# Performance work log

Measured on AMD Instinct MI355X. Metric: run time of the kernel, lower is better.

## Reference

```python
import jax, jax.numpy as jnp
import numpy as np
import math

D_MODEL = 512
N_HEADS = 8
PATH_LEN = 3
B, L, S = 4, 1024, 1024


def _path_index_structure(L, S, path_length):
    """Precompute the static multi-hop index structure (numpy, trace-time)."""
    i = np.arange(L)[:, None]          # [L,1]
    j = np.arange(S)[None, :]          # [1,S]
    step = (j - i) / path_length       # float
    # Python int() truncates toward zero; i + k*step >= 0 here, so floor == int().
    m1 = np.floor(i + 1 * step).astype(np.int32)  # [L,S] first intermediate point
    m2 = np.floor(i + 2 * step).astype(np.int32)  # [L,S] second intermediate point
    near = np.abs(i - j) <= path_length            # [L,S] bool: direct-score region
    return m1, m2, near


def setup_inputs() -> dict:
    key = jax.random.key(0)
    ks = jax.random.split(key, 7)
    inp = {
        "queries": jax.random.normal(ks[0], (B, L, D_MODEL), dtype=jnp.float32),
        "keys": jax.random.normal(ks[1], (B, S, D_MODEL), dtype=jnp.float32),
        "values": jax.random.normal(ks[2], (B, S, D_MODEL), dtype=jnp.float32),
        # nn.Linear(d_model, d_keys*n_heads, bias=False): stored as [in, out] so y = x @ W
        "W_q": jax.random.normal(ks[3], (D_MODEL, D_MODEL), dtype=jnp.float32) * 0.02,
        "W_k": jax.random.normal(ks[4], (D_MODEL, D_MODEL), dtype=jnp.float32) * 0.02,
        "W_v": jax.random.normal(ks[5], (D_MODEL, D_MODEL), dtype=jnp.float32) * 0.02,
        "W_o": jax.random.normal(ks[6], (D_MODEL, D_MODEL), dtype=jnp.float32) * 0.02,
    }
    return inp


def reference(queries, keys, values, W_q, W_k, W_v, W_o):
    Bv, Lv, _ = queries.shape
    Sv = keys.shape[1]
    H = N_HEADS
    q = (queries @ W_q).reshape(Bv, Lv, H, -1).transpose(0, 2, 1, 3)  # [B,H,L,D]
    k = (keys @ W_k).reshape(Bv, Sv, H, -1).transpose(0, 2, 1, 3)     # [B,H,S,D]
    v = (values @ W_v).reshape(Bv, Sv, H, -1).transpose(0, 2, 1, 3)   # [B,H,S,D]
    D = q.shape[-1]

    scores = jnp.einsum('bhld,bhsd->bhls', q, k) / math.sqrt(D)  # [B,H,L,S]

    # --- path-score modification (vectorized form of the nested loops) ---
    m1, m2, near = _path_index_structure(Lv, Sv, PATH_LEN)
    row = np.arange(Lv)[:, None]
    col = np.arange(Sv)[None, :]
    a = scores[:, :, row, m1]   # scores[:,:,i,m1(i,j)] -> [B,H,L,S]
    b = scores[:, :, m2, col]   # scores[:,:,m2(i,j),j] -> [B,H,L,S]
    # .mean() in the original reduces over BOTH batch and heads to a scalar per (i,j)
    path_mean = jnp.mean(a * b, axis=(0, 1))  # [L,S]
    scores = jnp.where(jnp.asarray(near), scores, path_mean[None, None, :, :])

    attn = jax.nn.softmax(scores, axis=-1)  # dropout p=0 in eval reference
    out = jnp.einsum('bhls,bhsd->blhd', attn, v).reshape(Bv, Lv, H * D)
    out = out @ W_o  # [B,L,d_model]
    return out, attn
```

## Files before the change

kernel.cpp:

```cpp
#include <hip/hip_runtime.h>
#include <math.h>

static constexpr int B_ = 4;
static constexpr int L_ = 1024;
static constexpr int S_ = 1024;
static constexpr int DMODEL = 512;
static constexpr int NH = 8;
static constexpr int DH = 64;
static constexpr int NBH = 32;

typedef __attribute__((ext_vector_type(8))) short s8;
typedef __attribute__((ext_vector_type(4))) float floatx4;

__device__ __forceinline__ short f2bf(float f) {
  unsigned u = __float_as_uint(f);
  return (short)((u + 0x7fffu + ((u >> 16) & 1u)) >> 16);
}
__device__ __forceinline__ float bf2f(short s) {
  return __uint_as_float(((unsigned)(unsigned short)s) << 16);
}

__global__ __launch_bounds__(256)
void cvt_inputs_kernel(const float* __restrict__ q, const float* __restrict__ k,
                       const float* __restrict__ v, short* __restrict__ dst,
                       float* __restrict__ bandS) {
  const int i = blockIdx.x * 256 + threadIdx.x;
  if (i < 32768) {
    const float4 m4 = make_float4(-1e30f, -1e30f, -1e30f, -1e30f);
    *(float4*)(bandS + ((size_t)i << 3)) = m4;
    *(float4*)(bandS + ((size_t)i << 3) + 4) = m4;
  }
  const int arr = i >> 18;
  const int off = (i & 262143) << 3;
  const float* src = (arr == 0) ? q : (arr == 1) ? k : v;
  const float4 f0 = *(const float4*)(src + off);
  const float4 f1 = *(const float4*)(src + off + 4);
  s8 o;
  o[0] = f2bf(f0.x); o[1] = f2bf(f0.y); o[2] = f2bf(f0.z); o[3] = f2bf(f0.w);
  o[4] = f2bf(f1.x); o[5] = f2bf(f1.y); o[6] = f2bf(f1.z); o[7] = f2bf(f1.w);
  *(s8*)(dst + (size_t)arr * 2097152 + off) = o;
}

__global__ __launch_bounds__(256)
void wtrans_kernel(const float* __restrict__ Wq, const float* __restrict__ Wk,
                   const float* __restrict__ Wv, const float* __restrict__ Wo,
                   short* __restrict__ WT) {
  __shared__ float t[32][33];
  const int z = blockIdx.z;
  const float* W = (z == 0) ? Wq : (z == 1) ? Wk : (z == 2) ? Wv : Wo;
  short* dst = WT + (size_t)z * 262144;
  const int k0 = blockIdx.y * 32, n0 = blockIdx.x * 32;
  const int row = threadIdx.x >> 3;
  const int c4 = (threadIdx.x & 7) << 2;
  const float4 f = *(const float4*)(W + (size_t)(k0 + row) * 512 + n0 + c4);
  t[row][c4 + 0] = f.x; t[row][c4 + 1] = f.y; t[row][c4 + 2] = f.z; t[row][c4 + 3] = f.w;
  __syncthreads();
#pragma unroll
  for (int j = 0; j < 4; ++j)
    dst[(size_t)(n0 + row) * 512 + k0 + c4 + j] = f2bf(t[c4 + j][row]);
}

__global__ __launch_bounds__(256)
void proj_qkv_kernel(const short* __restrict__ xbf, const short* __restrict__ WTall,
                     short* __restrict__ qk, short* __restrict__ vT,
                     short* __restrict__ vS) {
  const int z = blockIdx.z;
  const short* A = xbf + (size_t)z * 2097152;
  const short* WT = WTall + (size_t)z * 262144;
  const int K = DMODEL;
  const int tid = threadIdx.x;
  const int lane = tid & 63, w = tid >> 6;
  const int wm = w >> 1, wn = w & 1;
  const int m0 = blockIdx.y * 64, n0 = blockIdx.x * 64;
  const int kl = (lane >> 4) << 3;
  const short* pA = A + (size_t)(m0 + wm * 32 + (lane & 15)) * K + kl;
  const short* pB = WT + (size_t)(n0 + wn * 32 + (lane & 15)) * K + kl;
  const size_t f16K = (size_t)16 * K;
  floatx4 acc00 = {0,0,0,0}, acc01 = {0,0,0,0}, acc10 = {0,0,0,0}, acc11 = {0,0,0,0};
  for (int k = 0; k < K; k += 32) {
    const s8 a0 = *(const s8*)(pA + k);
    const s8 a1 = *(const s8*)(pA + f16K + k);
    const s8 b0 = *(const s8*)(pB + k);
    const s8 b1 = *(const s8*)(pB + f16K + k);
    acc00 = __builtin_amdgcn_mfma_f32_16x16x32_bf16(a0, b0, acc00, 0, 0, 0);
    acc01 = __builtin_amdgcn_mfma_f32_16x16x32_bf16(a0, b1, acc01, 0, 0, 0);
    acc10 = __builtin_amdgcn_mfma_f32_16x16x32_bf16(a1, b0, acc10, 0, 0, 0);
    acc11 = __builtin_amdgcn_mfma_f32_16x16x32_bf16(a1, b1, acc11, 0, 0, 0);
  }
  const int crow = (lane >> 4) << 2;
  const int ccol = lane & 15;
#pragma unroll
  for (int fm = 0; fm < 2; ++fm)
#pragma unroll
    for (int fn = 0; fn < 2; ++fn) {
      const floatx4 acc = (fm == 0) ? ((fn == 0) ? acc00 : acc01)
                                    : ((fn == 0) ? acc10 : acc11);
      const int col = n0 + wn * 32 + fn * 16 + ccol;
#pragma unroll
      for (int r = 0; r < 4; ++r) {
        const int row = m0 + wm * 32 + fm * 16 + crow + r;
        const int b = row >> 10, l = row & 1023, h = col >> 6, d = col & 63;
        const short val = f2bf(acc[r]);
        if (z < 2) {
          qk[(size_t)z * 2097152 + ((size_t)((b * NH + h) * L_ + l)) * DH + d] = val;
        } else {
          vT[((size_t)((b * NH + h) * DH + d)) * S_ + l] = val;
          vS[((size_t)((b * NH + h) * S_ + l)) * DH + d] = val;
        }
      }
    }
}

__global__ __launch_bounds__(256)
void scores_bf16_kernel(const short* __restrict__ qbf, const short* __restrict__ kbf,
                        short* __restrict__ Sbf, float* __restrict__ bandS) {
  const int tid = threadIdx.x;
  const int lane = tid & 63, w = tid >> 6;
  const int wm = w >> 1, wn = w & 1;
  const int m0 = blockIdx.y * 64, n0 = blockIdx.x * 64;
  const int bh = blockIdx.z;
  const int kl = (lane >> 4) << 3;
  const short* pA = qbf + (size_t)bh * L_ * DH + (size_t)(m0 + wm * 32 + (lane & 15)) * DH + kl;
  const short* pB = kbf + (size_t)bh * S_ * DH + (size_t)(n0 + wn * 32 + (lane & 15)) * DH + kl;
  floatx4 acc00 = {0,0,0,0}, acc01 = {0,0,0,0}, acc10 = {0,0,0,0}, acc11 = {0,0,0,0};
#pragma unroll
  for (int k = 0; k < DH; k += 32) {
    const s8 a0 = *(const s8*)(pA + k);
    const s8 a1 = *(const s8*)(pA + 16 * DH + k);
    const s8 b0 = *(const s8*)(pB + k);
    const s8 b1 = *(const s8*)(pB + 16 * DH + k);
    acc00 = __builtin_amdgcn_mfma_f32_16x16x32_bf16(a0, b0, acc00, 0, 0, 0);
    acc01 = __builtin_amdgcn_mfma_f32_16x16x32_bf16(a0, b1, acc01, 0, 0, 0);
    acc10 = __builtin_amdgcn_mfma_f32_16x16x32_bf16(a1, b0, acc10, 0, 0, 0);
    acc11 = __builtin_amdgcn_mfma_f32_16x16x32_bf16(a1, b1, acc11, 0, 0, 0);
  }
  short* Sp = Sbf + ((size_t)bh << 20);
  const int crow = (lane >> 4) << 2;
  const int ccol = lane & 15;
#pragma unroll
  for (int fm = 0; fm < 2; ++fm)
#pragma unroll
    for (int fn = 0; fn < 2; ++fn) {
      const floatx4 acc = (fm == 0) ? ((fn == 0) ? acc00 : acc01)
                                    : ((fn == 0) ? acc10 : acc11);
      const int col = n0 + wn * 32 + fn * 16 + ccol;
#pragma unroll
      for (int r = 0; r < 4; ++r) {
        const int row = m0 + wm * 32 + fm * 16 + crow + r;
        const float sc = acc[r] * 0.125f;
        Sp[(size_t)row * S_ + col] = f2bf(sc);
        const int dd = col - row;
        if (dd >= -3 && dd <= 3)
          bandS[(((size_t)bh << 10) + row) * 8 + dd + 3] = sc;
      }
    }
}

__global__ __launch_bounds__(256)
void path_mean_kernel(const short* __restrict__ Sbf, float* __restrict__ pm) {
  __shared__ float As[32][44];
  __shared__ float Bs[32][36];
  const int orig = blockIdx.x;
  const int wgid = (orig & 7) * 128 + (orig >> 3);
  const int i0 = (wgid >> 5) << 5;
  const int j0 = (wgid & 31) << 5;
  const int c0 = (2 * i0 + j0) / 3;
  const int c0a = c0 & ~7;
  const int r0 = (i0 + 2 * j0) / 3;
  const int tid = threadIdx.x;
  const int ti = tid >> 3;
  const int tj = tid & 7;
  const int gi = i0 + ti;
  int aoff[4], boff[4];
#pragma unroll
  for (int b = 0; b < 4; ++b) {
    const int gj = j0 + 4 * tj + b;
    const int m1 = (2 * gi + gj) / 3;
    const int m2 = (gi + 2 * gj) / 3;
    aoff[b] = ti * 44 + (m1 - c0a);
    boff[b] = (m2 - r0) * 36 + (4 * tj + b);
  }
  const int uA = tid;
  const int uB2 = tid + 256;
  int arow = 0, ac = 0, brow = 0, bc = 0, brow2 = 0, bc2 = 0;
  bool isA = uA < 160;
  if (isA) { arow = uA / 5; ac = uA - arow * 5; }
  else { const int v = uA - 160; brow = v >> 2; bc = v & 3; }
  const bool hasU2 = tid < 32;
  { const int v = uB2 - 160; brow2 = v >> 2; bc2 = v & 3; }
  int gcA = c0a + (ac << 3); if (gcA > 1016) gcA = 1016;
  const short* pA = Sbf + (size_t)(i0 + arow) * S_ + gcA;
  const short* pB = Sbf + (size_t)(r0 + brow) * S_ + j0 + (bc << 3);
  const short* pB2 = Sbf + (size_t)(r0 + brow2) * S_ + j0 + (bc2 << 3);

  const float* As0 = &As[0][0];
  const float* Bs0 = &Bs[0][0];
  float acc[4] = {0.f, 0.f, 0.f, 0.f};
  for (int z = 0; z < NBH; ++z) {
    const size_t zo = (size_t)z << 20;
    const s8 v1 = isA ? *(const s8*)(pA + zo) : *(const s8*)(pB + zo);
    s8 v2;
    if (hasU2) v2 = *(const s8*)(pB2 + zo);
    __syncthreads();
    {
      float4 lo, hi;
      lo.x = bf2f(v1[0]); lo.y = bf2f(v1[1]); lo.z = bf2f(v1[2]); lo.w = bf2f(v1[3]);
      hi.x = bf2f(v1[4]); hi.y = bf2f(v1[5]); hi.z = bf2f(v1[6]); hi.w = bf2f(v1[7]);
      if (isA) {
        *(float4*)&As[arow][ac << 3] = lo;
        *(float4*)&As[arow][(ac << 3) + 4] = hi;
      } else {
        *(float4*)&Bs[brow][bc << 3] = lo;
        *(float4*)&Bs[brow][(bc << 3) + 4] = hi;
      }
      if (hasU2) {
        float4 lo2, hi2;
        lo2.x = bf2f(v2[0]); lo2.y = bf2f(v2[1]); lo2.z = bf2f(v2[2]); lo2.w = bf2f(v2[3]);
        hi2.x = bf2f(v2[4]); hi2.y = bf2f(v2[5]); hi2.z = bf2f(v2[6]); hi2.w = bf2f(v2[7]);
        *(float4*)&Bs[brow2][bc2 << 3] = lo2;
        *(float4*)&Bs[brow2][(bc2 << 3) + 4] = hi2;
      }
    }
    __syncthreads();
#pragma unroll
    for (int b = 0; b < 4; ++b)
      acc[b] = fmaf(As0[aoff[b]], Bs0[boff[b]], acc[b]);
  }
  float4 o = make_float4(acc[0] * (1.f / 32.f), acc[1] * (1.f / 32.f),
                         acc[2] * (1.f / 32.f), acc[3] * (1.f / 32.f));
  *(float4*)&pm[(size_t)gi * S_ + j0 + 4 * tj] = o;
}

__global__ __launch_bounds__(256)
void pm_stats_kernel(const float* __restrict__ pm, short* __restrict__ E,
                     float* __restrict__ pmmax, float* __restrict__ pmsum) {
  const int wid = threadIdx.x >> 6, lane = threadIdx.x & 63;
  const int i = blockIdx.x * 4 + wid;
  const float* row = pm + (size_t)i * S_;
  const int j0 = lane << 4;
  float v[16];
#pragma unroll
  for (int c = 0; c < 4; ++c) {
    const float4 f = *(const float4*)(row + j0 + c * 4);
    v[c * 4 + 0] = f.x; v[c * 4 + 1] = f.y; v[c * 4 + 2] = f.z; v[c * 4 + 3] = f.w;
  }
  float mx = -1e30f;
#pragma unroll
  for (int u = 0; u < 16; ++u) {
    const int d = i - (j0 + u);
    const bool far = (d > 3) || (d < -3);
    if (far) mx = fmaxf(mx, v[u]);
  }
#pragma unroll
  for (int off = 32; off >= 1; off >>= 1) mx = fmaxf(mx, __shfl_xor(mx, off));
  float sum = 0.f;
  short e[16];
#pragma unroll
  for (int u = 0; u < 16; ++u) {
    const int d = i - (j0 + u);
    const bool far = (d > 3) || (d < -3);
    const float ev = far ? __expf(v[u] - mx) : 0.f;
    sum += ev;
    e[u] = f2bf(ev);
  }
#pragma unroll
  for (int off = 32; off >= 1; off >>= 1) sum += __shfl_xor(sum, off);
  s8 o0, o1;
#pragma unroll
  for (int u = 0; u < 8; ++u) { o0[u] = e[u]; o1[u] = e[8 + u]; }
  short* Erow = E + (size_t)i * S_ + j0;
  *(s8*)Erow = o0;
  *(s8*)(Erow + 8) = o1;
  if (lane == 0) { pmmax[i] = mx; pmsum[i] = sum; }
}

__global__ __launch_bounds__(256)
void ev_fused_kernel(const short* __restrict__ E, const short* __restrict__ vT,
                     const short* __restrict__ vS, const float* __restrict__ bandS,
                     const float* __restrict__ pmmax, const float* __restrict__ pmsum,
                     float* __restrict__ attn, short* __restrict__ out1) {
  __shared__ float cL[64];
  __shared__ float bL[64][8];
  __shared__ short Vb[70 * 64];
  const int tid = threadIdx.x;
  const int m0 = blockIdx.x * 64;
  const int bh = blockIdx.y;
  const int b = bh >> 3, h = bh & 7;

  for (int idx = tid; idx < 560; idx += 256) {
    const int rr = idx >> 3, c8 = (idx & 7) << 3;
    int j = m0 - 3 + rr; j = j < 0 ? 0 : (j > 1023 ? 1023 : j);
    *(s8*)&Vb[rr * 64 + c8] = *(const s8*)(vS + ((size_t)bh * S_ + j) * DH + c8);
  }

  {
    const int r = tid >> 2, p = tid & 3;
    const int l = m0 + r;
    const float pmx = pmmax[l], psum = pmsum[l];
    const float* bs = bandS + (((size_t)bh << 10) + l) * 8;
    const float sa = bs[p], sb2 = bs[p + 4];
    float mx = fmaxf(sa, sb2);
    mx = fmaxf(mx, __shfl_xor(mx, 1));
    mx = fmaxf(mx, __shfl_xor(mx, 2));
    const float m = fmaxf(mx, pmx);
    const float ea = __expf(sa - m), eb = __expf(sb2 - m);
    float bsum = ea + eb;
    bsum += __shfl_xor(bsum, 1);
    bsum += __shfl_xor(bsum, 2);
    const float cpm = __expf(pmx - m);
    const float inv = 1.f / (bsum + psum * cpm);
    if (p == 0) cL[r] = cpm * inv;
    bL[r][p] = ea * inv;
    bL[r][p + 4] = eb * inv;
  }
  __syncthreads();

  const int lane = tid & 63, w = tid >> 6;
  const int wm = w >> 1, wn = w & 1;
  const int frow = lane & 15;
  const int kl = (lane >> 4) << 3;
  const int ra0 = m0 + wm * 32 + frow;
  const int lr0 = wm * 32 + frow;
  const int lr1 = lr0 + 16;
  const short* pA = E + (size_t)ra0 * S_ + kl;
  const short* pB = vT + (size_t)bh * DH * S_ + (size_t)(wn * 32 + frow) * S_ + kl;
  const float c0v = cL[lr0];
  const float c1v = cL[lr1];
  float* arow0 = attn + ((size_t)bh * L_ + ra0) * S_;
  float* arow1 = arow0 + (size_t)16 * S_;
  floatx4 acc00 = {0,0,0,0}, acc01 = {0,0,0,0}, acc10 = {0,0,0,0}, acc11 = {0,0,0,0};
  for (int k = 0; k < S_; k += 32) {
    const s8 a0 = *(const s8*)(pA + k);
    const s8 a1 = *(const s8*)(pA + 16 * S_ + k);
    const s8 b0 = *(const s8*)(pB + k);
    const s8 b1 = *(const s8*)(pB + 16 * S_ + k);
    acc00 = __builtin_amdgcn_mfma_f32_16x16x32_bf16(a0, b0, acc00, 0, 0, 0);
    acc01 = __builtin_amdgcn_mfma_f32_16x16x32_bf16(a0, b1, acc01, 0, 0, 0);
    acc10 = __builtin_amdgcn_mfma_f32_16x16x32_bf16(a1, b0, acc10, 0, 0, 0);
    acc11 = __builtin_amdgcn_mfma_f32_16x16x32_bf16(a1, b1, acc11, 0, 0, 0);
    const int jw = k + kl;
    if (wn == 0) {
      float att[8];
#pragma unroll
      for (int e = 0; e < 8; ++e) att[e] = bf2f(a0[e]) * c0v;
      const int rel = ra0 - jw;
      if ((unsigned)(rel + 3) <= 13u) {
#pragma unroll
        for (int e = 0; e < 8; ++e) {
          const int d = e - rel;
          if ((unsigned)(d + 3) <= 6u) att[e] = bL[lr0][d + 3];
        }
      }
      *(float4*)(arow0 + jw) = make_float4(att[0], att[1], att[2], att[3]);
      *(float4*)(arow0 + jw + 4) = make_float4(att[4], att[5], att[6], att[7]);
    } else {
      float att[8];
#pragma unroll
      for (int e = 0; e < 8; ++e) att[e] = bf2f(a1[e]) * c1v;
      const int rel = ra0 + 16 - jw;
      if ((unsigned)(rel + 3) <= 13u) {
#pragma unroll
        for (int e = 0; e < 8; ++e) {
          const int d = e - rel;
          if ((unsigned)(d + 3) <= 6u) att[e] = bL[lr1][d + 3];
        }
      }
      *(float4*)(arow1 + jw) = make_float4(att[0], att[1], att[2], att[3]);
      *(float4*)(arow1 + jw + 4) = make_float4(att[4], att[5], att[6], att[7]);
    }
  }

  const int crow = (lane >> 4) << 2;
  const int ccol = lane & 15;
#pragma unroll
  for (int fm = 0; fm < 2; ++fm)
#pragma unroll
    for (int r = 0; r < 4; ++r) {
      const int lrel = wm * 32 + fm * 16 + crow + r;
      const int l = m0 + lrel;
      const float cc = cL[lrel];
      const float4 b0v = *(const float4*)&bL[lrel][0];
      const float4 b1v = *(const float4*)&bL[lrel][4];
      const float bav[7] = {b0v.x, b0v.y, b0v.z, b0v.w, b1v.x, b1v.y, b1v.z};
#pragma unroll
      for (int fn = 0; fn < 2; ++fn) {
        const floatx4 acc = (fm == 0) ? ((fn == 0) ? acc00 : acc01)
                                      : ((fn == 0) ? acc10 : acc11);
        const int d = wn * 32 + fn * 16 + ccol;
        float corr = 0.f;
#pragma unroll
        for (int u = 0; u < 7; ++u)
          corr = fmaf(bav[u], bf2f(Vb[(lrel + u) * 64 + d]), corr);
        const float val = fmaf(cc, acc[r], corr);
        out1[((size_t)(b * L_ + l)) * DMODEL + h * DH + d] = f2bf(val);
      }
    }
}

__global__ __launch_bounds__(256)
void proj_out_kernel(const short* __restrict__ A, const short* __restrict__ WT,
                     float* __restrict__ C) {
  const int K = DMODEL;
  const int tid = threadIdx.x;
  const int lane = tid & 63, w = tid >> 6;
  const int wm = w >> 1, wn = w & 1;
  const int m0 = blockIdx.y * 64, n0 = blockIdx.x * 64;
  const int kl = (lane >> 4) << 3;
  const short* pA = A + (size_t)(m0 + wm * 32 + (lane & 15)) * K + kl;
  const short* pB = WT + (size_t)(n0 + wn * 32 + (lane & 15)) * K + kl;
  const size_t f16K = (size_t)16 * K;
  floatx4 acc00 = {0,0,0,0}, acc01 = {0,0,0,0}, acc10 = {0,0,0,0}, acc11 = {0,0,0,0};
  for (int k = 0; k < K; k += 32) {
    const s8 a0 = *(const s8*)(pA + k);
    const s8 a1 = *(const s8*)(pA + f16K + k);
    const s8 b0 = *(const s8*)(pB + k);
    const s8 b1 = *(const s8*)(pB + f16K + k);
    acc00 = __builtin_amdgcn_mfma_f32_16x16x32_bf16(a0, b0, acc00, 0, 0, 0);
    acc01 = __builtin_amdgcn_mfma_f32_16x16x32_bf16(a0, b1, acc01, 0, 0, 0);
    acc10 = __builtin_amdgcn_mfma_f32_16x16x32_bf16(a1, b0, acc10, 0, 0, 0);
    acc11 = __builtin_amdgcn_mfma_f32_16x16x32_bf16(a1, b1, acc11, 0, 0, 0);
  }
  const int crow = (lane >> 4) << 2;
  const int ccol = lane & 15;
#pragma unroll
  for (int fm = 0; fm < 2; ++fm)
#pragma unroll
    for (int fn = 0; fn < 2; ++fn) {
      const floatx4 acc = (fm == 0) ? ((fn == 0) ? acc00 : acc01)
                                    : ((fn == 0) ? acc10 : acc11);
      const int col = n0 + wn * 32 + fn * 16 + ccol;
#pragma unroll
      for (int r = 0; r < 4; ++r) {
        const int row = m0 + wm * 32 + fm * 16 + crow + r;
        C[(size_t)row * DMODEL + col] = acc[r];
      }
    }
}

extern "C" void kernel_launch(void* const* d_in, const int* in_sizes, int n_in,
                              void* d_out, int out_size, void* d_ws, size_t ws_size,
                              hipStream_t stream) {
  const float* queries = (const float*)d_in[0];
  const float* keys    = (const float*)d_in[1];
  const float* values  = (const float*)d_in[2];
  const float* Wq      = (const float*)d_in[3];
  const float* Wk      = (const float*)d_in[4];
  const float* Wv      = (const float*)d_in[5];
  const float* Wo      = (const float*)d_in[6];

  float* out  = (float*)d_out;
  float* attn = out + (size_t)B_ * L_ * DMODEL;

  char* ws = (char*)d_ws;
  short* xbf   = (short*)(ws);
  short* WT    = (short*)(ws + 12u * 1048576);
  short* qkbf  = (short*)(ws + 14u * 1048576);
  short* vT    = (short*)(ws + 22u * 1048576);
  short* vS    = (short*)(ws + 26u * 1048576);
  float* pm    = (float*)(ws + 30u * 1048576);
  short* E     = (short*)(ws + 34u * 1048576);
  float* pmmax = (float*)(ws + 36u * 1048576);
  float* pmsum = (float*)(ws + 36u * 1048576 + 4096);
  float* bandS = (float*)(ws + 37u * 1048576);
  short* out1  = (short*)(ws + 38u * 1048576);
  short* Sbf   = (short*)(ws + 42u * 1048576);

  const dim3 blk(256);

  hipLaunchKernelGGL(cvt_inputs_kernel, dim3(3072), blk, 0, stream,
                     queries, keys, values, xbf, bandS);
  hipLaunchKernelGGL(wtrans_kernel, dim3(16, 16, 4), blk, 0, stream,
                     Wq, Wk, Wv, Wo, WT);

  hipLaunchKernelGGL(proj_qkv_kernel, dim3(DMODEL / 64, (B_ * L_) / 64, 3),
                     blk, 0, stream, xbf, WT, qkbf, vT, vS);

  hipLaunchKernelGGL(scores_bf16_kernel, dim3(S_ / 64, L_ / 64, NBH), blk, 0, stream,
                     qkbf, qkbf + 2097152, Sbf, bandS);

  hipLaunchKernelGGL(path_mean_kernel, dim3(1024), blk, 0, stream, Sbf, pm);

  hipLaunchKernelGGL(pm_stats_kernel, dim3(L_ / 4), blk, 0, stream,
                     pm, E, pmmax, pmsum);

  hipLaunchKernelGGL(ev_fused_kernel, dim3(L_ / 64, NBH), blk, 0, stream,
                     E, vT, vS, bandS, pmmax, pmsum, attn, out1);

  hipLaunchKernelGGL(proj_out_kernel, dim3(DMODEL / 64, (B_ * L_) / 64), blk, 0, stream,
                     out1, WT + 786432, out);
}
```

Before: 202.2 us.

## Stage GEMM epilogues through LDS for coalesced stores and merge prep kernels

Merges the input conversion and weight transpose kernels into one launch. The q/k projection, scores, ev_fused and output projection epilogues now write their accumulator tiles to shared memory first, then issue 16-byte coalesced row stores instead of scattered 2- or 4-byte stores. The attention matrix stores become nontemporal. This removes one launch and makes global writes much more efficient, at the cost of extra LDS space and a barrier in each kernel.

```diff
diff --git a/kernel.cpp b/kernel.cpp
--- a/kernel.cpp
+++ b/kernel.cpp
@@ -21,49 +21,52 @@
 }
 
 __global__ __launch_bounds__(256)
-void cvt_inputs_kernel(const float* __restrict__ q, const float* __restrict__ k,
-                       const float* __restrict__ v, short* __restrict__ dst,
-                       float* __restrict__ bandS) {
-  const int i = blockIdx.x * 256 + threadIdx.x;
-  if (i < 32768) {
-    const float4 m4 = make_float4(-1e30f, -1e30f, -1e30f, -1e30f);
-    *(float4*)(bandS + ((size_t)i << 3)) = m4;
-    *(float4*)(bandS + ((size_t)i << 3) + 4) = m4;
-  }
-  const int arr = i >> 18;
-  const int off = (i & 262143) << 3;
-  const float* src = (arr == 0) ? q : (arr == 1) ? k : v;
-  const float4 f0 = *(const float4*)(src + off);
-  const float4 f1 = *(const float4*)(src + off + 4);
-  s8 o;
-  o[0] = f2bf(f0.x); o[1] = f2bf(f0.y); o[2] = f2bf(f0.z); o[3] = f2bf(f0.w);
-  o[4] = f2bf(f1.x); o[5] = f2bf(f1.y); o[6] = f2bf(f1.z); o[7] = f2bf(f1.w);
-  *(s8*)(dst + (size_t)arr * 2097152 + off) = o;
-}
-
-__global__ __launch_bounds__(256)
-void wtrans_kernel(const float* __restrict__ Wq, const float* __restrict__ Wk,
-                   const float* __restrict__ Wv, const float* __restrict__ Wo,
-                   short* __restrict__ WT) {
+void prep_kernel(const float* __restrict__ q, const float* __restrict__ k,
+                 const float* __restrict__ v, short* __restrict__ dst,
+                 float* __restrict__ bandS,
+                 const float* __restrict__ Wq, const float* __restrict__ Wk,
+                 const float* __restrict__ Wv, const float* __restrict__ Wo,
+                 short* __restrict__ WT) {
   __shared__ float t[32][33];
-  const int z = blockIdx.z;
-  const float* W = (z == 0) ? Wq : (z == 1) ? Wk : (z == 2) ? Wv : Wo;
-  short* dst = WT + (size_t)z * 262144;
-  const int k0 = blockIdx.y * 32, n0 = blockIdx.x * 32;
-  const int row = threadIdx.x >> 3;
-  const int c4 = (threadIdx.x & 7) << 2;
-  const float4 f = *(const float4*)(W + (size_t)(k0 + row) * 512 + n0 + c4);
-  t[row][c4 + 0] = f.x; t[row][c4 + 1] = f.y; t[row][c4 + 2] = f.z; t[row][c4 + 3] = f.w;
-  __syncthreads();
-#pragma unroll
-  for (int j = 0; j < 4; ++j)
-    dst[(size_t)(n0 + row) * 512 + k0 + c4 + j] = f2bf(t[c4 + j][row]);
+  if (blockIdx.x < 3072) {
+    const int i = blockIdx.x * 256 + threadIdx.x;
+    if (i < 32768) {
+      const float4 m4 = make_float4(-1e30f, -1e30f, -1e30f, -1e30f);
+      *(float4*)(bandS + ((size_t)i << 3)) = m4;
+      *(float4*)(bandS + ((size_t)i << 3) + 4) = m4;
+    }
+    const int arr = i >> 18;
+    const int off = (i & 262143) << 3;
+    const float* src = (arr == 0) ? q : (arr == 1) ? k : v;
+    const float4 f0 = *(const float4*)(src + off);
+    const float4 f1 = *(const float4*)(src + off + 4);
+    s8 o;
+    o[0] = f2bf(f0.x); o[1] = f2bf(f0.y); o[2] = f2bf(f0.z); o[3] = f2bf(f0.w);
+    o[4] = f2bf(f1.x); o[5] = f2bf(f1.y); o[6] = f2bf(f1.z); o[7] = f2bf(f1.w);
+    *(s8*)(dst + (size_t)arr * 2097152 + off) = o;
+  } else {
+    const int bid2 = blockIdx.x - 3072;
+    const int z = bid2 >> 8;
+    const int rem = bid2 & 255;
+    const int k0 = (rem >> 4) << 5, n0 = (rem & 15) << 5;
+    const float* W = (z == 0) ? Wq : (z == 1) ? Wk : (z == 2) ? Wv : Wo;
+    short* dw = WT + (size_t)z * 262144;
+    const int row = threadIdx.x >> 3;
+    const int c4 = (threadIdx.x & 7) << 2;
+    const float4 f = *(const float4*)(W + (size_t)(k0 + row) * 512 + n0 + c4);
+    t[row][c4 + 0] = f.x; t[row][c4 + 1] = f.y; t[row][c4 + 2] = f.z; t[row][c4 + 3] = f.w;
+    __syncthreads();
+#pragma unroll
+    for (int j = 0; j < 4; ++j)
+      dw[(size_t)(n0 + row) * 512 + k0 + c4 + j] = f2bf(t[c4 + j][row]);
+  }
 }
 
 __global__ __launch_bounds__(256)
 void proj_qkv_kernel(const short* __restrict__ xbf, const short* __restrict__ WTall,
                      short* __restrict__ qk, short* __restrict__ vT,
                      short* __restrict__ vS) {
+  __shared__ short tileS[64][72];
   const int z = blockIdx.z;
   const short* A = xbf + (size_t)z * 2097152;
   const short* WT = WTall + (size_t)z * 262144;
@@ -89,31 +92,50 @@
   }
   const int crow = (lane >> 4) << 2;
   const int ccol = lane & 15;
-#pragma unroll
-  for (int fm = 0; fm < 2; ++fm)
-#pragma unroll
-    for (int fn = 0; fn < 2; ++fn) {
-      const floatx4 acc = (fm == 0) ? ((fn == 0) ? acc00 : acc01)
-                                    : ((fn == 0) ? acc10 : acc11);
-      const int col = n0 + wn * 32 + fn * 16 + ccol;
-#pragma unroll
-      for (int r = 0; r < 4; ++r) {
-        const int row = m0 + wm * 32 + fm * 16 + crow + r;
-        const int b = row >> 10, l = row & 1023, h = col >> 6, d = col & 63;
-        const short val = f2bf(acc[r]);
-        if (z < 2) {
-          qk[(size_t)z * 2097152 + ((size_t)((b * NH + h) * L_ + l)) * DH + d] = val;
-        } else {
+  if (z < 2) {
+#pragma unroll
+    for (int fm = 0; fm < 2; ++fm)
+#pragma unroll
+      for (int fn = 0; fn < 2; ++fn) {
+        const floatx4 acc = (fm == 0) ? ((fn == 0) ? acc00 : acc01)
+                                      : ((fn == 0) ? acc10 : acc11);
+#pragma unroll
+        for (int r = 0; r < 4; ++r)
+          tileS[wm * 32 + fm * 16 + crow + r][wn * 32 + fn * 16 + ccol] = f2bf(acc[r]);
+      }
+    __syncthreads();
+    const int b = m0 >> 10, l0 = m0 & 1023, h = n0 >> 6;
+    short* base = qk + (size_t)z * 2097152 + ((size_t)((b * NH + h) * L_ + l0)) * DH;
+#pragma unroll
+    for (int qk2 = 0; qk2 < 2; ++qk2) {
+      const int c = tid + qk2 * 256;
+      const int row = c >> 3, off = (c & 7) << 3;
+      *(s8*)(base + (size_t)row * DH + off) = *(const s8*)&tileS[row][off];
+    }
+  } else {
+#pragma unroll
+    for (int fm = 0; fm < 2; ++fm)
+#pragma unroll
+      for (int fn = 0; fn < 2; ++fn) {
+        const floatx4 acc = (fm == 0) ? ((fn == 0) ? acc00 : acc01)
+                                      : ((fn == 0) ? acc10 : acc11);
+        const int col = n0 + wn * 32 + fn * 16 + ccol;
+#pragma unroll
+        for (int r = 0; r < 4; ++r) {
+          const int row = m0 + wm * 32 + fm * 16 + crow + r;
+          const int b = row >> 10, l = row & 1023, h = col >> 6, d = col & 63;
+          const short val = f2bf(acc[r]);
           vT[((size_t)((b * NH + h) * DH + d)) * S_ + l] = val;
           vS[((size_t)((b * NH + h) * S_ + l)) * DH + d] = val;
         }
       }
-    }
+  }
 }
 
 __global__ __launch_bounds__(256)
 void scores_bf16_kernel(const short* __restrict__ qbf, const short* __restrict__ kbf,
                         short* __restrict__ Sbf, float* __restrict__ bandS) {
+  __shared__ short tileS[64][72];
   const int tid = threadIdx.x;
   const int lane = tid & 63, w = tid >> 6;
   const int wm = w >> 1, wn = w & 1;
@@ -134,7 +156,6 @@
     acc10 = __builtin_amdgcn_mfma_f32_16x16x32_bf16(a1, b0, acc10, 0, 0, 0);
     acc11 = __builtin_amdgcn_mfma_f32_16x16x32_bf16(a1, b1, acc11, 0, 0, 0);
   }
-  short* Sp = Sbf + ((size_t)bh << 20);
   const int crow = (lane >> 4) << 2;
   const int ccol = lane & 15;
 #pragma unroll
@@ -148,12 +169,20 @@
       for (int r = 0; r < 4; ++r) {
         const int row = m0 + wm * 32 + fm * 16 + crow + r;
         const float sc = acc[r] * 0.125f;
-        Sp[(size_t)row * S_ + col] = f2bf(sc);
+        tileS[wm * 32 + fm * 16 + crow + r][wn * 32 + fn * 16 + ccol] = f2bf(sc);
         const int dd = col - row;
         if (dd >= -3 && dd <= 3)
           bandS[(((size_t)bh << 10) + row) * 8 + dd + 3] = sc;
       }
     }
+  __syncthreads();
+  short* Sp = Sbf + ((size_t)bh << 20) + (size_t)m0 * S_ + n0;
+#pragma unroll
+  for (int q2 = 0; q2 < 2; ++q2) {
+    const int c = tid + q2 * 256;
+    const int row = c >> 3, off = (c & 7) << 3;
+    *(s8*)(Sp + (size_t)row * S_ + off) = *(const s8*)&tileS[row][off];
+  }
 }
 
 __global__ __launch_bounds__(256)
@@ -282,6 +311,7 @@
   __shared__ float cL[64];
   __shared__ float bL[64][8];
   __shared__ short Vb[70 * 64];
+  __shared__ short tileO[64][72];
   const int tid = threadIdx.x;
   const int m0 = blockIdx.x * 64;
   const int bh = blockIdx.y;
@@ -351,8 +381,10 @@
           if ((unsigned)(d + 3) <= 6u) att[e] = bL[lr0][d + 3];
         }
       }
-      *(float4*)(arow0 + jw) = make_float4(att[0], att[1], att[2], att[3]);
-      *(float4*)(arow0 + jw + 4) = make_float4(att[4], att[5], att[6], att[7]);
+      floatx4 v0 = {att[0], att[1], att[2], att[3]};
+      floatx4 v1 = {att[4], att[5], att[6], att[7]};
+      __builtin_nontemporal_store(v0, (floatx4*)(arow0 + jw));
+      __builtin_nontemporal_store(v1, (floatx4*)(arow0 + jw + 4));
     } else {
       float att[8];
 #pragma unroll
@@ -365,8 +397,10 @@
           if ((unsigned)(d + 3) <= 6u) att[e] = bL[lr1][d + 3];
         }
       }
-      *(float4*)(arow1 + jw) = make_float4(att[0], att[1], att[2], att[3]);
-      *(float4*)(arow1 + jw + 4) = make_float4(att[4], att[5], att[6], att[7]);
+      floatx4 v0 = {att[0], att[1], att[2], att[3]};
+      floatx4 v1 = {att[4], att[5], att[6], att[7]};
+      __builtin_nontemporal_store(v0, (floatx4*)(arow1 + jw));
+      __builtin_nontemporal_store(v1, (floatx4*)(arow1 + jw + 4));
     }
   }
 
@@ -377,7 +411,6 @@
 #pragma unroll
     for (int r = 0; r < 4; ++r) {
       const int lrel = wm * 32 + fm * 16 + crow + r;
-      const int l = m0 + lrel;
       const float cc = cL[lrel];
       const float4 b0v = *(const float4*)&bL[lrel][0];
       const float4 b1v = *(const float4*)&bL[lrel][4];
@@ -391,15 +424,23 @@
 #pragma unroll
         for (int u = 0; u < 7; ++u)
           corr = fmaf(bav[u], bf2f(Vb[(lrel + u) * 64 + d]), corr);
-        const float val = fmaf(cc, acc[r], corr);
-        out1[((size_t)(b * L_ + l)) * DMODEL + h * DH + d] = f2bf(val);
-      }
-    }
+        tileO[lrel][d] = f2bf(fmaf(cc, acc[r], corr));
+      }
+    }
+  __syncthreads();
+  short* obase = out1 + ((size_t)(b * L_ + m0)) * DMODEL + h * DH;
+#pragma unroll
+  for (int q2 = 0; q2 < 2; ++q2) {
+    const int c = tid + q2 * 256;
+    const int row = c >> 3, off = (c & 7) << 3;
+    *(s8*)(obase + (size_t)row * DMODEL + off) = *(const s8*)&tileO[row][off];
+  }
 }
 
 __global__ __launch_bounds__(256)
 void proj_out_kernel(const short* __restrict__ A, const short* __restrict__ WT,
                      float* __restrict__ C) {
+  __shared__ float tileF[64][68];
   const int K = DMODEL;
   const int tid = threadIdx.x;
   const int lane = tid & 63, w = tid >> 6;
@@ -428,13 +469,18 @@
     for (int fn = 0; fn < 2; ++fn) {
       const floatx4 acc = (fm == 0) ? ((fn == 0) ? acc00 : acc01)
                                     : ((fn == 0) ? acc10 : acc11);
-      const int col = n0 + wn * 32 + fn * 16 + ccol;
-#pragma unroll
-      for (int r = 0; r < 4; ++r) {
-        const int row = m0 + wm * 32 + fm * 16 + crow + r;
-        C[(size_t)row * DMODEL + col] = acc[r];
-      }
-    }
+#pragma unroll
+      for (int r = 0; r < 4; ++r)
+        tileF[wm * 32 + fm * 16 + crow + r][wn * 32 + fn * 16 + ccol] = acc[r];
+    }
+  __syncthreads();
+  float* base = C + (size_t)m0 * DMODEL + n0;
+#pragma unroll
+  for (int q2 = 0; q2 < 4; ++q2) {
+    const int c = tid + q2 * 256;
+    const int row = c >> 4, off = (c & 15) << 2;
+    *(float4*)(base + (size_t)row * DMODEL + off) = *(const float4*)&tileF[row][off];
+  }
 }
 
 extern "C" void kernel_launch(void* const* d_in, const int* in_sizes, int n_in,
@@ -467,10 +513,8 @@
 
   const dim3 blk(256);
 
-  hipLaunchKernelGGL(cvt_inputs_kernel, dim3(3072), blk, 0, stream,
-                     queries, keys, values, xbf, bandS);
-  hipLaunchKernelGGL(wtrans_kernel, dim3(16, 16, 4), blk, 0, stream,
-                     Wq, Wk, Wv, Wo, WT);
+  hipLaunchKernelGGL(prep_kernel, dim3(4096), blk, 0, stream,
+                     queries, keys, values, xbf, bandS, Wq, Wk, Wv, Wo, WT);
 
   hipLaunchKernelGGL(proj_qkv_kernel, dim3(DMODEL / 64, (B_ * L_) / 64, 3),
                      blk, 0, stream, xbf, WT, qkbf, vT, vS);
```

Result: no change. 203.3 us (+0.5%).
